# Optimization experiments

Measured on AMD Instinct MI355X. Metric: run time of the kernel, lower is better.

## Reference

```python
import jax, jax.numpy as jnp
import numpy as np

N_NODES = 50000
N_EDGES = 800000
IN_DIM = 1200   # latent_size * num_heads
OUT_DIM = 300
NEG_SLOPE = 0.2  # PyG GATConv default


def setup_inputs() -> dict:
    key = jax.random.key(0)
    k1, k2, k3, k4, k5 = jax.random.split(key, 5)
    z = jax.random.normal(k1, (N_NODES, IN_DIM), dtype=jnp.float32)
    edge_index = jax.random.randint(k2, (2, N_EDGES), 0, N_NODES, dtype=jnp.int64)
    # GATConv params (heads=1): lin weight [out, in], attention vectors [out], bias [out]
    W = jax.random.normal(k3, (OUT_DIM, IN_DIM), dtype=jnp.float32) * (1.0 / np.sqrt(IN_DIM))
    att_src = jax.random.normal(k4, (OUT_DIM,), dtype=jnp.float32) * 0.1
    att_dst = jax.random.normal(k5, (OUT_DIM,), dtype=jnp.float32) * 0.1
    bias = jnp.zeros((OUT_DIM,), dtype=jnp.float32)
    return {"z": z, "edge_index": edge_index, "W": W,
            "att_src": att_src, "att_dst": att_dst, "bias": bias}


def reference(z, edge_index, W, att_src, att_dst, bias):
    N = z.shape[0]
    # Linear projection (no bias on lin in GATConv; bias added after aggregation)
    x = z @ W.T                                   # [N, OUT_DIM]
    # add self-loops (GATConv default add_self_loops=True)
    loop = jnp.arange(N, dtype=edge_index.dtype)
    src = jnp.concatenate([edge_index[0], loop])  # message source j
    dst = jnp.concatenate([edge_index[1], loop])  # message target i
    # per-node attention logits
    a_src = x @ att_src                           # [N]
    a_dst = x @ att_dst                           # [N]
    # per-edge score, softmax over incoming edges of each target node
    e = jax.nn.leaky_relu(a_src[src] + a_dst[dst], negative_slope=NEG_SLOPE)  # [E+N]
    e_max = jax.ops.segment_max(e, dst, num_segments=N)   # every node has a self-loop
    ex = jnp.exp(e - e_max[dst])
    denom = jax.ops.segment_sum(ex, dst, num_segments=N)
    alpha = ex / denom[dst]                       # [E+N]
    # weighted aggregation (scatter-add over targets)
    out = jax.ops.segment_sum(alpha[:, None] * x[src], dst, num_segments=N)
    return out + bias
```

## Files before the change

kernel.cpp:

```cpp
#include <hip/hip_runtime.h>

#define N_NODES 50000
#define N_EDGES 800000
#define IN_DIM  1200
#define KP      1216
#define OUT_DIM 300
#define BNP     320
#define XBS     304
#define BM      128
#define NKT     38
#define GRID_M  ((N_NODES + BM - 1) / BM)

typedef __attribute__((ext_vector_type(8))) short short8;
typedef __attribute__((ext_vector_type(4))) float f32x4;

__device__ __forceinline__ short f2bf(float f) {
  unsigned u = __builtin_bit_cast(unsigned, f);
  u += 0x7fffu + ((u >> 16) & 1u);
  return (short)(u >> 16);
}
__device__ __forceinline__ float bf2f(unsigned short h) {
  return __builtin_bit_cast(float, (unsigned)h << 16);
}
__device__ __forceinline__ float lrelu(float v) { return v > 0.f ? v : 0.2f * v; }

__device__ __forceinline__ float wredMaxF(float v) {
  #pragma unroll
  for (int o = 32; o > 0; o >>= 1) v = fmaxf(v, __shfl_xor(v, o));
  return v;
}
__device__ __forceinline__ float wredSumF(float v) {
  #pragma unroll
  for (int o = 32; o > 0; o >>= 1) v += __shfl_xor(v, o);
  return v;
}

__device__ __forceinline__ void gl_lds16(const unsigned short* g, unsigned short* l) {
  __builtin_amdgcn_global_load_lds(
      (const __attribute__((address_space(1))) unsigned int*)g,
      (__attribute__((address_space(3))) unsigned int*)l, 16, 0, 0);
}

__global__ __launch_bounds__(256) void wconv(const float* __restrict__ W,
                                             unsigned short* __restrict__ Wb) {
  int f = blockIdx.x * 256 + threadIdx.x;
  if (f >= BNP * KP / 8) return;
  int n = (f * 8) / KP, c = (f * 8) % KP;
  short8 v = {0,0,0,0,0,0,0,0};
  if (n < OUT_DIM && c < IN_DIM) {
    const float4* p = reinterpret_cast<const float4*>(W + (size_t)n * IN_DIM + c);
    float4 f0 = p[0], f1 = p[1];
    v[0]=f2bf(f0.x); v[1]=f2bf(f0.y); v[2]=f2bf(f0.z); v[3]=f2bf(f0.w);
    v[4]=f2bf(f1.x); v[5]=f2bf(f1.y); v[6]=f2bf(f1.z); v[7]=f2bf(f1.w);
  }
  *reinterpret_cast<short8*>(&Wb[(size_t)n * KP + c]) = v;
}

__global__ __launch_bounds__(512) void gemm_x(const float* __restrict__ z,
                                              const unsigned short* __restrict__ Wb,
                                              const float* __restrict__ att_s,
                                              const float* __restrict__ att_d,
                                              unsigned short* __restrict__ xb,
                                              float* __restrict__ a_s,
                                              float* __restrict__ a_d) {
  __shared__ __align__(16) unsigned short As[2][BM * 32];
  __shared__ __align__(16) unsigned short Bs[2][BNP * 32];

  const int tid  = threadIdx.x;
  const int lane = tid & 63;
  const int wid  = tid >> 6;
  const int mw   = wid >> 2;
  const int nw   = wid & 3;
  const int lr   = lane & 15;
  const int lg   = lane >> 4;
  const int lrs  = (lr >> 1) & 3;
  const int m0   = blockIdx.x * BM;

  f32x4 zero4 = {0.f, 0.f, 0.f, 0.f};
  const float4 fz4 = make_float4(0.f, 0.f, 0.f, 0.f);
  f32x4 acc[4][5];
  #pragma unroll
  for (int mf = 0; mf < 4; ++mf)
    #pragma unroll
    for (int nj = 0; nj < 5; ++nj) acc[mf][nj] = zero4;

  const int ra  = tid >> 2;
  const int kaL = tid & 3;
  const int kaP = kaL ^ ((ra >> 1) & 3);
  const int am  = m0 + ra;
  float4 ga0, ga1;

  const int bgc = (lane & 3) ^ ((lane >> 3) & 3);

  #define LOADA(KT)                                                           \
    {                                                                         \
      int k = (KT) * 32 + kaL * 8;                                            \
      if (am < N_NODES && k + 8 <= IN_DIM) {                                  \
        const float4* p = reinterpret_cast<const float4*>(z + (size_t)am * IN_DIM + k); \
        ga0 = p[0]; ga1 = p[1];                                               \
      } else { ga0 = fz4; ga1 = fz4; }                                        \
    }

  #define WRITEA(BUF)                                                         \
    {                                                                         \
      short8 v;                                                               \
      v[0]=f2bf(ga0.x); v[1]=f2bf(ga0.y); v[2]=f2bf(ga0.z); v[3]=f2bf(ga0.w); \
      v[4]=f2bf(ga1.x); v[5]=f2bf(ga1.y); v[6]=f2bf(ga1.z); v[7]=f2bf(ga1.w); \
      *reinterpret_cast<short8*>(&As[BUF][ra * 32 + kaP * 8]) = v;            \
    }

  #define STAGEB(BUF, KT)                                                     \
    _Pragma("unroll")                                                         \
    for (int t5 = 0; t5 < 3; ++t5) {                                          \
      int j = wid + 8 * t5;                                                   \
      if (j < 20) {                                                           \
        const unsigned short* gsrc =                                          \
            Wb + (size_t)(j * 16 + (lane >> 2)) * KP + (KT) * 32 + bgc * 8;   \
        gl_lds16(gsrc, &Bs[BUF][j * 16 * 32]);                                \
      }                                                                       \
    }

  STAGEB(0, 0);
  LOADA(0);
  WRITEA(0);
  __syncthreads();

  #pragma unroll 1
  for (int kt = 0; kt < NKT; ++kt) {
    const int cur = kt & 1;
    if (kt < NKT - 1) {
      STAGEB(cur ^ 1, kt + 1);
      LOADA(kt + 1);
    }

    short8 a0 = *reinterpret_cast<const short8*>(&As[cur][(mw * 64 +      lr) * 32 + (lg ^ lrs) * 8]);
    short8 a1 = *reinterpret_cast<const short8*>(&As[cur][(mw * 64 + 16 + lr) * 32 + (lg ^ lrs) * 8]);
    short8 a2 = *reinterpret_cast<const short8*>(&As[cur][(mw * 64 + 32 + lr) * 32 + (lg ^ lrs) * 8]);
    short8 a3 = *reinterpret_cast<const short8*>(&As[cur][(mw * 64 + 48 + lr) * 32 + (lg ^ lrs) * 8]);
    #pragma unroll
    for (int nj = 0; nj < 5; ++nj) {
      short8 b = *reinterpret_cast<const short8*>(
          &Bs[cur][(nw * 80 + nj * 16 + lr) * 32 + (lg ^ lrs) * 8]);
      acc[0][nj] = __builtin_amdgcn_mfma_f32_16x16x32_bf16(a0, b, acc[0][nj], 0, 0, 0);
      acc[1][nj] = __builtin_amdgcn_mfma_f32_16x16x32_bf16(a1, b, acc[1][nj], 0, 0, 0);
      acc[2][nj] = __builtin_amdgcn_mfma_f32_16x16x32_bf16(a2, b, acc[2][nj], 0, 0, 0);
      acc[3][nj] = __builtin_amdgcn_mfma_f32_16x16x32_bf16(a3, b, acc[3][nj], 0, 0, 0);
    }

    if (kt < NKT - 1) { WRITEA(cur ^ 1); }
    __syncthreads();
  }
  #undef LOADA
  #undef WRITEA
  #undef STAGEB

  float* red = reinterpret_cast<float*>(&As[0][0]);

  float ps[4][4], pd[4][4];
  #pragma unroll
  for (int mf = 0; mf < 4; ++mf)
    #pragma unroll
    for (int jj = 0; jj < 4; ++jj) { ps[mf][jj] = 0.f; pd[mf][jj] = 0.f; }

  #pragma unroll
  for (int nj = 0; nj < 5; ++nj) {
    int c = nw * 80 + nj * 16 + lr;
    bool cv = c < OUT_DIM;
    float vs = cv ? att_s[c] : 0.f;
    float vd = cv ? att_d[c] : 0.f;
    #pragma unroll
    for (int mf = 0; mf < 4; ++mf) {
      #pragma unroll
      for (int jj = 0; jj < 4; ++jj) {
        float val = acc[mf][nj][jj];
        int r = m0 + mw * 64 + mf * 16 + 4 * lg + jj;
        if (cv && r < N_NODES) xb[(size_t)r * XBS + c] = (unsigned short)f2bf(val);
        ps[mf][jj] += val * vs;
        pd[mf][jj] += val * vd;
      }
    }
  }
  #pragma unroll
  for (int mf = 0; mf < 4; ++mf)
    #pragma unroll
    for (int jj = 0; jj < 4; ++jj) {
      #pragma unroll
      for (int o = 8; o > 0; o >>= 1) {
        ps[mf][jj] += __shfl_xor(ps[mf][jj], o);
        pd[mf][jj] += __shfl_xor(pd[mf][jj], o);
      }
      if (lr == 0) {
        int rr = mw * 64 + mf * 16 + 4 * lg + jj;
        red[nw * 128 + rr]       = ps[mf][jj];
        red[512 + nw * 128 + rr] = pd[mf][jj];
      }
    }
  __syncthreads();
  if (tid < 128) {
    int r = m0 + tid;
    if (r < N_NODES)
      a_s[r] = red[tid] + red[128 + tid] + red[256 + tid] + red[384 + tid];
  } else if (tid < 256) {
    int t = tid - 128, r = m0 + t;
    if (r < N_NODES)
      a_d[r] = red[512 + t] + red[512 + 128 + t] + red[512 + 256 + t] + red[512 + 384 + t];
  }
}

__global__ void hist(const int* __restrict__ ei, int* __restrict__ deg) {
  int e = blockIdx.x * blockDim.x + threadIdx.x;
  if (e < N_EDGES) {
    unsigned dst = (unsigned)ei[N_EDGES + e];
    if (dst < N_NODES) atomicAdd(&deg[dst], 1);
  }
}

#define SCAN_B 1024
#define NBLK   49

__global__ __launch_bounds__(SCAN_B) void scan1(const int* __restrict__ deg,
                                                int* __restrict__ bsum) {
  int i = blockIdx.x * SCAN_B + threadIdx.x;
  int v = (i < N_NODES) ? deg[i] : 0;
  #pragma unroll
  for (int o = 32; o > 0; o >>= 1) v += __shfl_xor(v, o);
  __shared__ int wt[16];
  if ((threadIdx.x & 63) == 0) wt[threadIdx.x >> 6] = v;
  __syncthreads();
  if (threadIdx.x == 0) {
    int t = 0;
    #pragma unroll
    for (int w = 0; w < 16; ++w) t += wt[w];
    bsum[blockIdx.x] = t;
  }
}

__global__ void scan2(const int* __restrict__ bsum, int* __restrict__ bex,
                      int* __restrict__ offs) {
  int l = threadIdx.x;
  int v = (l < NBLK) ? bsum[l] : 0;
  int incl = v;
  #pragma unroll
  for (int off = 1; off < 64; off <<= 1) {
    int u = __shfl_up(incl, off);
    if (l >= off) incl += u;
  }
  if (l < NBLK) bex[l] = incl - v;
  if (l == NBLK - 1) offs[N_NODES] = incl;
}

__global__ __launch_bounds__(SCAN_B) void scan3(const int* __restrict__ deg,
                                                const int* __restrict__ bex,
                                                int* __restrict__ offs,
                                                int* __restrict__ cursor) {
  int tid = threadIdx.x;
  int i = blockIdx.x * SCAN_B + tid;
  int lane = tid & 63, wid = tid >> 6;
  int v = (i < N_NODES) ? deg[i] : 0;
  int incl = v;
  #pragma unroll
  for (int off = 1; off < 64; off <<= 1) {
    int u = __shfl_up(incl, off);
    if (lane >= off) incl += u;
  }
  __shared__ int wt[16];
  if (lane == 63) wt[wid] = incl;
  __syncthreads();
  if (tid < 16) {
    int t = wt[tid];
    int sc = t;
    #pragma unroll
    for (int off = 1; off < 16; off <<= 1) {
      int u = __shfl_up(sc, off);
      if (tid >= off) sc += u;
    }
    wt[tid] = sc - t;
  }
  __syncthreads();
  int excl = incl - v + wt[wid] + bex[blockIdx.x];
  if (i < N_NODES) { offs[i] = excl; cursor[i] = excl; }
}

__global__ void fill(const int* __restrict__ ei, int* __restrict__ cursor,
                     int* __restrict__ srcs) {
  int e = blockIdx.x * blockDim.x + threadIdx.x;
  if (e < N_EDGES) {
    unsigned dst = (unsigned)ei[N_EDGES + e];
    unsigned src = (unsigned)ei[e];
    if (dst < N_NODES && src < N_NODES) {
      int pos = atomicAdd(&cursor[dst], 1);
      srcs[pos] = (int)src;
    }
  }
}

__global__ __launch_bounds__(256) void minv_k(const float* __restrict__ a_s,
                                              const float* __restrict__ a_d,
                                              const int* __restrict__ offs,
                                              const int* __restrict__ srcs,
                                              float2* __restrict__ minv) {
  int node = blockIdx.x * 4 + (threadIdx.x >> 6);
  if (node >= N_NODES) return;
  int lane = threadIdx.x & 63;
  int beg = offs[node], end = offs[node + 1];
  float adi = a_d[node];
  float eself = lrelu(a_s[node] + adi);

  float m = eself;
  for (int k = beg + lane; k < end; k += 64)
    m = fmaxf(m, lrelu(a_s[srcs[k]] + adi));
  m = wredMaxF(m);

  float s = 0.f;
  for (int k = beg + lane; k < end; k += 64)
    s += expf(lrelu(a_s[srcs[k]] + adi) - m);
  s = wredSumF(s) + expf(eself - m);
  if (lane == 0) minv[node] = make_float2(m, 1.0f / s);
}

#define CCH 15
__global__ __launch_bounds__(256) void aggregate(const unsigned short* __restrict__ xb,
                                                 const float* __restrict__ a_s,
                                                 const float* __restrict__ a_d,
                                                 const float2* __restrict__ minv,
                                                 const int* __restrict__ offs,
                                                 const int* __restrict__ srcs,
                                                 const float* __restrict__ bias,
                                                 float* __restrict__ out) {
  unsigned wi = blockIdx.x * 256u + threadIdx.x;
  if (wi >= (unsigned)N_NODES * CCH) return;
  unsigned node = wi / CCH;
  unsigned cc = wi - node * CCH;

  int beg = offs[node], end = offs[node + 1];
  float2 mi = minv[node];
  const float m = mi.x, inv = mi.y;
  const float adi = a_d[node];
  const float wself = expf(lrelu(a_s[node] + adi) - m) * inv;

  const unsigned short* xcol = xb + 20u * cc;

  float acc[20];
  {
    const unsigned short* xr = xcol + (size_t)node * XBS;
    #pragma unroll
    for (int q = 0; q < 5; ++q) {
      ushort4 xv = *reinterpret_cast<const ushort4*>(xr + 4 * q);
      acc[4*q+0] = wself * bf2f(xv.x);
      acc[4*q+1] = wself * bf2f(xv.y);
      acc[4*q+2] = wself * bf2f(xv.z);
      acc[4*q+3] = wself * bf2f(xv.w);
    }
  }

  for (int k = beg; k < end; ++k) {
    int sj = srcs[k];
    float w = expf(lrelu(a_s[sj] + adi) - m) * inv;
    const unsigned short* xr = xcol + (size_t)sj * XBS;
    #pragma unroll
    for (int q = 0; q < 5; ++q) {
      ushort4 xv = *reinterpret_cast<const ushort4*>(xr + 4 * q);
      acc[4*q+0] += w * bf2f(xv.x);
      acc[4*q+1] += w * bf2f(xv.y);
      acc[4*q+2] += w * bf2f(xv.z);
      acc[4*q+3] += w * bf2f(xv.w);
    }
  }
  float* op = out + (size_t)node * OUT_DIM + 20u * cc;
  const float* bp = bias + 20u * cc;
  #pragma unroll
  for (int q = 0; q < 5; ++q) {
    float4 b = *reinterpret_cast<const float4*>(bp + 4 * q);
    float4 o = {acc[4*q] + b.x, acc[4*q+1] + b.y, acc[4*q+2] + b.z, acc[4*q+3] + b.w};
    *reinterpret_cast<float4*>(op + 4 * q) = o;
  }
}

extern "C" void kernel_launch(void* const* d_in, const int* in_sizes, int n_in,
                              void* d_out, int out_size, void* d_ws, size_t ws_size,
                              hipStream_t stream) {
  const float* z     = (const float*)d_in[0];
  const int*   ei    = (const int*)d_in[1];
  const float* W     = (const float*)d_in[2];
  const float* att_s = (const float*)d_in[3];
  const float* att_d = (const float*)d_in[4];
  const float* bias  = (const float*)d_in[5];
  float* out = (float*)d_out;

  char* ws = (char*)d_ws;
  size_t off = 0;
  unsigned short* xb = (unsigned short*)(ws + off); off += (size_t)N_NODES * XBS * 2;
  unsigned short* Wb = (unsigned short*)(ws + off); off += (size_t)BNP * KP * 2;
  float*  a_s  = (float*)(ws + off);  off += 50048 * 4;
  float*  a_d  = (float*)(ws + off);  off += 50048 * 4;
  int*    deg  = (int*)(ws + off);    off += 50048 * 4;
  int*    offs = (int*)(ws + off);    off += 50056 * 4;
  int*    cur  = (int*)(ws + off);    off += 50048 * 4;
  int*    bsum = (int*)(ws + off);    off += 64 * 4;
  int*    bex  = (int*)(ws + off);    off += 64 * 4;
  int*    srcs = (int*)(ws + off);    off += (size_t)N_EDGES * 4;
  float2* minv = (float2*)(ws + off); off += (size_t)50048 * 8;

  (void)hipMemsetAsync(deg, 0, N_NODES * 4, stream);

  wconv<<<(BNP * KP / 8 + 255) / 256, 256, 0, stream>>>(W, Wb);
  gemm_x<<<GRID_M, 512, 0, stream>>>(z, Wb, att_s, att_d, xb, a_s, a_d);
  hist<<<(N_EDGES + 255) / 256, 256, 0, stream>>>(ei, deg);
  scan1<<<NBLK, SCAN_B, 0, stream>>>(deg, bsum);
  scan2<<<1, 64, 0, stream>>>(bsum, bex, offs);
  scan3<<<NBLK, SCAN_B, 0, stream>>>(deg, bex, offs, cur);
  fill<<<(N_EDGES + 255) / 256, 256, 0, stream>>>(ei, cur, srcs);
  minv_k<<<(N_NODES + 3) / 4, 256, 0, stream>>>(a_s, a_d, offs, srcs, minv);
  aggregate<<<((unsigned)N_NODES * CCH + 255) / 256, 256, 0, stream>>>(
      xb, a_s, a_d, minv, offs, srcs, bias, out);
}
```

Baseline: 332.0 us.

## Fuse softmax statistics into aggregation with one wavefront per node

Merges the separate max/denominator kernel into the aggregation kernel, so one 64-lane wavefront per node computes the softmax max and sum and then gathers neighbor rows. Each lane now loads 8 bf16 values with a 16-byte load (38 active lanes cover 304 columns) instead of 15 threads per node each loading 20 columns. This removes a kernel launch and the minv round trip, and makes the neighbor-row gathers coalesced per wavefront. In exchange, 26 of 64 lanes sit idle during aggregation and each wave handles only one node, which lowers useful occupancy.

```diff
diff --git a/kernel.cpp b/kernel.cpp
--- a/kernel.cpp
+++ b/kernel.cpp
@@ -294,17 +294,19 @@
   }
 }
 
-__global__ __launch_bounds__(256) void minv_k(const float* __restrict__ a_s,
-                                              const float* __restrict__ a_d,
-                                              const int* __restrict__ offs,
-                                              const int* __restrict__ srcs,
-                                              float2* __restrict__ minv) {
-  int node = blockIdx.x * 4 + (threadIdx.x >> 6);
+__global__ __launch_bounds__(256) void aggregate(const unsigned short* __restrict__ xb,
+                                                 const float* __restrict__ a_s,
+                                                 const float* __restrict__ a_d,
+                                                 const int* __restrict__ offs,
+                                                 const int* __restrict__ srcs,
+                                                 const float* __restrict__ bias,
+                                                 float* __restrict__ out) {
+  const int node = blockIdx.x * 4 + (threadIdx.x >> 6);
   if (node >= N_NODES) return;
-  int lane = threadIdx.x & 63;
-  int beg = offs[node], end = offs[node + 1];
-  float adi = a_d[node];
-  float eself = lrelu(a_s[node] + adi);
+  const int lane = threadIdx.x & 63;
+  const int beg = offs[node], end = offs[node + 1];
+  const float adi = a_d[node];
+  const float eself = lrelu(a_s[node] + adi);
 
   float m = eself;
   for (int k = beg + lane; k < end; k += 64)
@@ -315,64 +317,44 @@
   for (int k = beg + lane; k < end; k += 64)
     s += expf(lrelu(a_s[srcs[k]] + adi) - m);
   s = wredSumF(s) + expf(eself - m);
-  if (lane == 0) minv[node] = make_float2(m, 1.0f / s);
-}
-
-#define CCH 15
-__global__ __launch_bounds__(256) void aggregate(const unsigned short* __restrict__ xb,
-                                                 const float* __restrict__ a_s,
-                                                 const float* __restrict__ a_d,
-                                                 const float2* __restrict__ minv,
-                                                 const int* __restrict__ offs,
-                                                 const int* __restrict__ srcs,
-                                                 const float* __restrict__ bias,
-                                                 float* __restrict__ out) {
-  unsigned wi = blockIdx.x * 256u + threadIdx.x;
-  if (wi >= (unsigned)N_NODES * CCH) return;
-  unsigned node = wi / CCH;
-  unsigned cc = wi - node * CCH;
-
-  int beg = offs[node], end = offs[node + 1];
-  float2 mi = minv[node];
-  const float m = mi.x, inv = mi.y;
-  const float adi = a_d[node];
-  const float wself = expf(lrelu(a_s[node] + adi) - m) * inv;
-
-  const unsigned short* xcol = xb + 20u * cc;
-
-  float acc[20];
+  const float inv = 1.0f / s;
+  const float wself = expf(eself - m) * inv;
+
+  const bool gl = lane < 38;
+  const unsigned short* xcol = xb + 8 * lane;
+
+  float acc[8];
   {
-    const unsigned short* xr = xcol + (size_t)node * XBS;
-    #pragma unroll
-    for (int q = 0; q < 5; ++q) {
-      ushort4 xv = *reinterpret_cast<const ushort4*>(xr + 4 * q);
-      acc[4*q+0] = wself * bf2f(xv.x);
-      acc[4*q+1] = wself * bf2f(xv.y);
-      acc[4*q+2] = wself * bf2f(xv.z);
-      acc[4*q+3] = wself * bf2f(xv.w);
-    }
+    short8 v = {0,0,0,0,0,0,0,0};
+    if (gl) v = *reinterpret_cast<const short8*>(xcol + (size_t)node * XBS);
+    #pragma unroll
+    for (int j = 0; j < 8; ++j) acc[j] = wself * bf2f((unsigned short)v[j]);
   }
 
   for (int k = beg; k < end; ++k) {
     int sj = srcs[k];
     float w = expf(lrelu(a_s[sj] + adi) - m) * inv;
-    const unsigned short* xr = xcol + (size_t)sj * XBS;
-    #pragma unroll
-    for (int q = 0; q < 5; ++q) {
-      ushort4 xv = *reinterpret_cast<const ushort4*>(xr + 4 * q);
-      acc[4*q+0] += w * bf2f(xv.x);
-      acc[4*q+1] += w * bf2f(xv.y);
-      acc[4*q+2] += w * bf2f(xv.z);
-      acc[4*q+3] += w * bf2f(xv.w);
-    }
-  }
-  float* op = out + (size_t)node * OUT_DIM + 20u * cc;
-  const float* bp = bias + 20u * cc;
-  #pragma unroll
-  for (int q = 0; q < 5; ++q) {
-    float4 b = *reinterpret_cast<const float4*>(bp + 4 * q);
-    float4 o = {acc[4*q] + b.x, acc[4*q+1] + b.y, acc[4*q+2] + b.z, acc[4*q+3] + b.w};
-    *reinterpret_cast<float4*>(op + 4 * q) = o;
+    short8 v = {0,0,0,0,0,0,0,0};
+    if (gl) v = *reinterpret_cast<const short8*>(xcol + (size_t)sj * XBS);
+    #pragma unroll
+    for (int j = 0; j < 8; ++j) acc[j] += w * bf2f((unsigned short)v[j]);
+  }
+
+  if (gl) {
+    float* op = out + (size_t)node * OUT_DIM + 8 * lane;
+    const float* bp = bias + 8 * lane;
+    if (lane < 37) {
+      float4 b0 = *reinterpret_cast<const float4*>(bp);
+      float4 b1 = *reinterpret_cast<const float4*>(bp + 4);
+      float4 o0 = {acc[0] + b0.x, acc[1] + b0.y, acc[2] + b0.z, acc[3] + b0.w};
+      float4 o1 = {acc[4] + b1.x, acc[5] + b1.y, acc[6] + b1.z, acc[7] + b1.w};
+      *reinterpret_cast<float4*>(op)     = o0;
+      *reinterpret_cast<float4*>(op + 4) = o1;
+    } else {
+      float4 b0 = *reinterpret_cast<const float4*>(bp);
+      float4 o0 = {acc[0] + b0.x, acc[1] + b0.y, acc[2] + b0.z, acc[3] + b0.w};
+      *reinterpret_cast<float4*>(op) = o0;
+    }
   }
 }
 
@@ -399,7 +381,6 @@
   int*    bsum = (int*)(ws + off);    off += 64 * 4;
   int*    bex  = (int*)(ws + off);    off += 64 * 4;
   int*    srcs = (int*)(ws + off);    off += (size_t)N_EDGES * 4;
-  float2* minv = (float2*)(ws + off); off += (size_t)50048 * 8;
 
   (void)hipMemsetAsync(deg, 0, N_NODES * 4, stream);
 
@@ -410,7 +391,5 @@
   scan2<<<1, 64, 0, stream>>>(bsum, bex, offs);
   scan3<<<NBLK, SCAN_B, 0, stream>>>(deg, bex, offs, cur);
   fill<<<(N_EDGES + 255) / 256, 256, 0, stream>>>(ei, cur, srcs);
-  minv_k<<<(N_NODES + 3) / 4, 256, 0, stream>>>(a_s, a_d, offs, srcs, minv);
-  aggregate<<<((unsigned)N_NODES * CCH + 255) / 256, 256, 0, stream>>>(
-      xb, a_s, a_d, minv, offs, srcs, bias, out);
-}
+  aggregate<<<(N_NODES + 3) / 4, 256, 0, stream>>>(xb, a_s, a_d, offs, srcs, bias, out);
+}
```

Result: slower. 347.1 us (+4.5%).

## Widen aggregate per-thread column chunk and vectorize edge-list kernels

Applied to the files above, without the earlier changes.

The aggregate kernel now gives each thread 64 output columns (5 chunks per node) instead of 20 (15 chunks). It gathers source rows with 16-byte short8 loads and guards the partial last chunk. This cuts how often each edge's srcs index, a_s lookup and exp weight are recomputed across threads, in exchange for 64 accumulator registers per thread and fewer threads in flight. The hist and fill kernels also handle four edges per thread with int4 loads to reduce per-edge index-load overhead.

```diff
diff --git a/kernel.cpp b/kernel.cpp
--- a/kernel.cpp
+++ b/kernel.cpp
@@ -208,10 +208,13 @@
 }
 
 __global__ void hist(const int* __restrict__ ei, int* __restrict__ deg) {
-  int e = blockIdx.x * blockDim.x + threadIdx.x;
-  if (e < N_EDGES) {
-    unsigned dst = (unsigned)ei[N_EDGES + e];
-    if (dst < N_NODES) atomicAdd(&deg[dst], 1);
+  int e4 = (blockIdx.x * blockDim.x + threadIdx.x) * 4;
+  if (e4 < N_EDGES) {
+    int4 d = *reinterpret_cast<const int4*>(ei + N_EDGES + e4);
+    if ((unsigned)d.x < N_NODES) atomicAdd(&deg[d.x], 1);
+    if ((unsigned)d.y < N_NODES) atomicAdd(&deg[d.y], 1);
+    if ((unsigned)d.z < N_NODES) atomicAdd(&deg[d.z], 1);
+    if ((unsigned)d.w < N_NODES) atomicAdd(&deg[d.w], 1);
   }
 }
 
@@ -283,14 +286,18 @@
 
 __global__ void fill(const int* __restrict__ ei, int* __restrict__ cursor,
                      int* __restrict__ srcs) {
-  int e = blockIdx.x * blockDim.x + threadIdx.x;
-  if (e < N_EDGES) {
-    unsigned dst = (unsigned)ei[N_EDGES + e];
-    unsigned src = (unsigned)ei[e];
-    if (dst < N_NODES && src < N_NODES) {
-      int pos = atomicAdd(&cursor[dst], 1);
-      srcs[pos] = (int)src;
-    }
+  int e4 = (blockIdx.x * blockDim.x + threadIdx.x) * 4;
+  if (e4 < N_EDGES) {
+    int4 s = *reinterpret_cast<const int4*>(ei + e4);
+    int4 d = *reinterpret_cast<const int4*>(ei + N_EDGES + e4);
+    if ((unsigned)d.x < N_NODES && (unsigned)s.x < N_NODES)
+      srcs[atomicAdd(&cursor[d.x], 1)] = s.x;
+    if ((unsigned)d.y < N_NODES && (unsigned)s.y < N_NODES)
+      srcs[atomicAdd(&cursor[d.y], 1)] = s.y;
+    if ((unsigned)d.z < N_NODES && (unsigned)s.z < N_NODES)
+      srcs[atomicAdd(&cursor[d.z], 1)] = s.z;
+    if ((unsigned)d.w < N_NODES && (unsigned)s.w < N_NODES)
+      srcs[atomicAdd(&cursor[d.w], 1)] = s.w;
   }
 }
 
@@ -318,7 +325,7 @@
   if (lane == 0) minv[node] = make_float2(m, 1.0f / s);
 }
 
-#define CCH 15
+#define CCH 5
 __global__ __launch_bounds__(256) void aggregate(const unsigned short* __restrict__ xb,
                                                  const float* __restrict__ a_s,
                                                  const float* __restrict__ a_d,
@@ -331,6 +338,7 @@
   if (wi >= (unsigned)N_NODES * CCH) return;
   unsigned node = wi / CCH;
   unsigned cc = wi - node * CCH;
+  const int col0 = 64 * (int)cc;
 
   int beg = offs[node], end = offs[node + 1];
   float2 mi = minv[node];
@@ -338,18 +346,17 @@
   const float adi = a_d[node];
   const float wself = expf(lrelu(a_s[node] + adi) - m) * inv;
 
-  const unsigned short* xcol = xb + 20u * cc;
-
-  float acc[20];
+  const unsigned short* xcol = xb + col0;
+
+  float acc[64];
   {
     const unsigned short* xr = xcol + (size_t)node * XBS;
     #pragma unroll
-    for (int q = 0; q < 5; ++q) {
-      ushort4 xv = *reinterpret_cast<const ushort4*>(xr + 4 * q);
-      acc[4*q+0] = wself * bf2f(xv.x);
-      acc[4*q+1] = wself * bf2f(xv.y);
-      acc[4*q+2] = wself * bf2f(xv.z);
-      acc[4*q+3] = wself * bf2f(xv.w);
+    for (int j = 0; j < 8; ++j) {
+      short8 v = {0,0,0,0,0,0,0,0};
+      if (col0 + 8 * j + 8 <= XBS) v = *reinterpret_cast<const short8*>(xr + 8 * j);
+      #pragma unroll
+      for (int q = 0; q < 8; ++q) acc[8*j+q] = wself * bf2f((unsigned short)v[q]);
     }
   }
 
@@ -358,21 +365,25 @@
     float w = expf(lrelu(a_s[sj] + adi) - m) * inv;
     const unsigned short* xr = xcol + (size_t)sj * XBS;
     #pragma unroll
-    for (int q = 0; q < 5; ++q) {
-      ushort4 xv = *reinterpret_cast<const ushort4*>(xr + 4 * q);
-      acc[4*q+0] += w * bf2f(xv.x);
-      acc[4*q+1] += w * bf2f(xv.y);
-      acc[4*q+2] += w * bf2f(xv.z);
-      acc[4*q+3] += w * bf2f(xv.w);
-    }
-  }
-  float* op = out + (size_t)node * OUT_DIM + 20u * cc;
-  const float* bp = bias + 20u * cc;
-  #pragma unroll
-  for (int q = 0; q < 5; ++q) {
-    float4 b = *reinterpret_cast<const float4*>(bp + 4 * q);
-    float4 o = {acc[4*q] + b.x, acc[4*q+1] + b.y, acc[4*q+2] + b.z, acc[4*q+3] + b.w};
-    *reinterpret_cast<float4*>(op + 4 * q) = o;
+    for (int j = 0; j < 8; ++j) {
+      if (col0 + 8 * j + 8 <= XBS) {
+        short8 v = *reinterpret_cast<const short8*>(xr + 8 * j);
+        #pragma unroll
+        for (int q = 0; q < 8; ++q) acc[8*j+q] += w * bf2f((unsigned short)v[q]);
+      }
+    }
+  }
+
+  float* op = out + (size_t)node * OUT_DIM + col0;
+  const float* bp = bias + col0;
+  #pragma unroll
+  for (int g = 0; g < 16; ++g) {
+    int c = col0 + 4 * g;
+    if (c + 4 <= OUT_DIM) {
+      float4 b = *reinterpret_cast<const float4*>(bp + 4 * g);
+      float4 o = {acc[4*g] + b.x, acc[4*g+1] + b.y, acc[4*g+2] + b.z, acc[4*g+3] + b.w};
+      *reinterpret_cast<float4*>(op + 4 * g) = o;
+    }
   }
 }
 
@@ -405,11 +416,11 @@
 
   wconv<<<(BNP * KP / 8 + 255) / 256, 256, 0, stream>>>(W, Wb);
   gemm_x<<<GRID_M, 512, 0, stream>>>(z, Wb, att_s, att_d, xb, a_s, a_d);
-  hist<<<(N_EDGES + 255) / 256, 256, 0, stream>>>(ei, deg);
+  hist<<<(N_EDGES / 4 + 255) / 256, 256, 0, stream>>>(ei, deg);
   scan1<<<NBLK, SCAN_B, 0, stream>>>(deg, bsum);
   scan2<<<1, 64, 0, stream>>>(bsum, bex, offs);
   scan3<<<NBLK, SCAN_B, 0, stream>>>(deg, bex, offs, cur);
-  fill<<<(N_EDGES + 255) / 256, 256, 0, stream>>>(ei, cur, srcs);
+  fill<<<(N_EDGES / 4 + 255) / 256, 256, 0, stream>>>(ei, cur, srcs);
   minv_k<<<(N_NODES + 3) / 4, 256, 0, stream>>>(a_s, a_d, offs, srcs, minv);
   aggregate<<<((unsigned)N_NODES * CCH + 255) / 256, 256, 0, stream>>>(
       xb, a_s, a_d, minv, offs, srcs, bias, out);
```

Result: slower. 442.5 us (+33.3%).
